# Performance work log

Hardware: AMD Instinct MI355X
Metric: run time of the kernel (lower is better)

Reference implementation:

```python
import jax, jax.numpy as jnp
import numpy as np

K = 15.0          # sigmoid sharpness in get_approxi
THETA2 = 400.0    # gaussian 'theta2' parameter
LOSS_WEIGHT = 1.0


def obb2poly_le90(boxes):
    # boxes [..., 5] = (x, y, w, h, a) -> poly [..., 8]
    x, y, w, h, a = (boxes[..., i] for i in range(5))
    cosa, sina = jnp.cos(a), jnp.sin(a)
    wx, wy = 0.5 * w * cosa, 0.5 * w * sina
    hx, hy = -0.5 * h * sina, 0.5 * h * cosa
    return jnp.stack([
        x - wx - hx, y - wy - hy,
        x + wx - hx, y + wy - hy,
        x + wx + hx, y + wy + hy,
        x - wx + hx, y - wy + hy,
    ], axis=-1)


def setup_inputs() -> dict:
    key = jax.random.key(0)
    k1, k2, k3, k4, k5, k6 = jax.random.split(key, 6)
    N, M = 256, 512

    def make_boxes(k):
        u = jax.random.uniform(k, (N, 5), dtype=jnp.float32)
        cx = 100.0 + 300.0 * u[:, 0]
        cy = 100.0 + 300.0 * u[:, 1]
        w = 20.0 + 100.0 * u[:, 2]
        h = 20.0 + 100.0 * u[:, 3]
        a = (u[:, 4] - 0.5) * (jnp.pi / 2)
        return jnp.stack([cx, cy, w, h, a], axis=-1)

    pred = make_boxes(k1)
    target = make_boxes(k2)
    mask = 512.0 * jax.random.uniform(k3, (N, M, 2), dtype=jnp.float32)
    grad_x = jax.random.normal(k4, (N, M), dtype=jnp.float32)
    grad_y = jax.random.normal(k5, (N, M), dtype=jnp.float32)
    offset = 50.0 * jax.random.uniform(k6, (N, 2), dtype=jnp.float32)
    return {"pred": pred, "target": target, "mask": mask,
            "grad_x": grad_x, "grad_y": grad_y, "offset": offset}


def _my_loss(pred, target, mask, grad_x, grad_y, offset):
    # pred/target [N,5], mask [N,M,2], grad_x/grad_y [N,M], offset [N,2]
    px = pred[:, 0] - offset[:, 0]   # [N]
    py = pred[:, 1] - offset[:, 1]
    pw, ph, pa = pred[:, 2], pred[:, 3], pred[:, 4]
    gx = target[:, 0] - offset[:, 0]
    gy = target[:, 1] - offset[:, 1]
    gw, gh, ga = target[:, 2], target[:, 3], target[:, 4]

    mx, my = mask[..., 0], mask[..., 1]            # [N,M]
    dx = mx - gx[:, None]
    dy = my - gy[:, None]
    d = jnp.sqrt(dx * dx + dy * dy)                # [N,M]
    acos_arg = jnp.clip((gx[:, None] - mx) / d, -1.0, 1.0)
    acosv = jnp.arccos(acos_arg)
    beta = jnp.where(gy[:, None] >= my, ga[:, None] + acosv, ga[:, None] - acosv)

    d_w = jnp.abs(d * jnp.cos(beta))
    d_h = jnp.abs(d * jnp.sin(beta))
    sig = jax.nn.sigmoid
    approxi_1 = (1.0 - sig(K * (d_w - gw[:, None]) / gw[:, None])) * \
                (1.0 - sig(K * (d_h - gh[:, None]) / gh[:, None]))  # [N,M]

    d_w_p = pw[:, None] * d_w / gw[:, None]
    d_h_p = ph[:, None] * d_h / gh[:, None]
    zeros = jnp.zeros_like(d_w_p)
    boxes = jnp.stack([zeros, zeros, 2.0 * d_w_p, 2.0 * d_h_p,
                       jnp.broadcast_to(pa[:, None], d_w_p.shape)], axis=-1)
    pts = obb2poly_le90(boxes)                     # [N,M,8]

    half_pi = jnp.pi / 2
    q2 = (beta > -half_pi) & (beta <= 0.0)
    q3 = (beta > -jnp.pi) & (beta <= -half_pi)
    q4 = (beta > half_pi) & (beta <= jnp.pi)
    # default (q1: 0 < beta <= pi/2) -> corner 0
    gpx = jnp.where(q2, pts[..., 2], jnp.where(q3, pts[..., 4], jnp.where(q4, pts[..., 6], pts[..., 0])))
    gpy = jnp.where(q2, pts[..., 3], jnp.where(q3, pts[..., 5], jnp.where(q4, pts[..., 7], pts[..., 1])))
    guass_x = px[:, None] + gpx                    # [N,M]
    guass_y = py[:, None] + gpy

    # approxi_2[n,i,j] = exp(+||guass_i - mask_j||^2 / (2*theta2^2)) / (2*pi*theta2)
    dgx = guass_x[:, :, None] - mx[:, None, :]
    dgy = guass_y[:, :, None] - my[:, None, :]
    approxi_2 = jnp.exp((dgx * dgx + dgy * dgy) / (2.0 * THETA2 * THETA2)) / (2.0 * jnp.pi * THETA2)

    # w[n,i,j] = gx_i*gx_j + gy_i*gy_j
    w = grad_x[:, :, None] * grad_x[:, None, :] + grad_y[:, :, None] * grad_y[:, None, :]

    loss_per_box = jnp.mean(w * approxi_2 * approxi_1[:, None, :], axis=(1, 2))  # [N]
    return loss_per_box


def reference(pred, target, mask, grad_x, grad_y, offset):
    loss_per_box = _my_loss(pred, target, mask, grad_x, grad_y, offset)
    return LOSS_WEIGHT * jnp.mean(loss_per_box)  # reduction='mean'
```

## Files before the change

### kernel.cpp

```cpp
#include <hip/hip_runtime.h>
#include <math.h>

typedef float v2f __attribute__((ext_vector_type(2)));

#define N_BOX   256
#define M_PTS   512
#define S_SPLIT 8
#define BLK_B   256
#define M2_PER  (M_PTS / S_SPLIT)
#define GRID_B  (N_BOX * S_SPLIT)


__global__ __launch_bounds__(512) void precompute(
    const float* __restrict__ pred,
    const float* __restrict__ target,
    const float* __restrict__ mask,
    const float* __restrict__ gradx,
    const float* __restrict__ grady,
    const float* __restrict__ offset,
    float4* __restrict__ P1,
    float4* __restrict__ P2)
{
    const int n = blockIdx.x;
    const int m = threadIdx.x;

    const float offx = offset[n * 2 + 0];
    const float offy = offset[n * 2 + 1];
    const float px = pred[n * 5 + 0] - offx;
    const float py = pred[n * 5 + 1] - offy;
    const float pw = pred[n * 5 + 2];
    const float ph = pred[n * 5 + 3];
    const float pa = pred[n * 5 + 4];
    const float gx = target[n * 5 + 0] - offx;
    const float gy = target[n * 5 + 1] - offy;
    const float gw = target[n * 5 + 2];
    const float gh = target[n * 5 + 3];
    const float ga = target[n * 5 + 4];

    float sinpa, cospa, singa, cosga;
    sincosf(pa, &sinpa, &cospa);
    sincosf(ga, &singa, &cosga);

    const float THETA2   = 400.0f;
    const float LOG2E    = 1.4426950408889634f;
    const float c1       = LOG2E / (2.0f * THETA2 * THETA2);
    const float rs       = sqrtf(c1);
    const float inv_norm = 1.0f / (2.0f * (float)M_PI * THETA2);

    const float pwg = pw / gw, phg = ph / gh;
    const float cwx = pwg * cospa, swx = pwg * sinpa;
    const float chx = phg * cospa, shx = phg * sinpa;
    const float absinga = fabsf(singa);
    const float kA  = 15.0f * LOG2E / gw;
    const float kH  = 15.0f * LOG2E / gh;
    const float kB  = 15.0f * LOG2E;
    const float pxrs = px * rs, pyrs = py * rs;
    const bool  gaPos = (ga > 0.0f), gaNeg = (ga < 0.0f);

    const float2* mask2 = (const float2*)mask;
    const size_t  idx   = (size_t)n * M_PTS + m;

    const float2 mp = mask2[idx];
    const float dx = mp.x - gx;
    const float dy = mp.y - gy;
    const float u = singa * dy - cosga * dx;
    const float v = -(cosga * dy + singa * dx);
    const bool sgaOk = gaPos ? (dy <= 0.0f) : (gaNeg ? (dy > 0.0f) : false);
    const bool wrap  = sgaOk && (dx > 0.0f) && (dx * absinga > fabsf(dy) * cosga);
    const float au = fabsf(u), av = fabsf(v);
    const float dws = (wrap || v > 0.0f) ? -au : au;
    const float dhs = (wrap || u > 0.0f) ? -av : av;
    const float gpx = dws * cwx - dhs * shx;
    const float gpy = dws * swx + dhs * chx;
    const float gvx = gradx[idx];
    const float gvy = grady[idx];

    const float eA = __builtin_amdgcn_exp2f(fmaf(au, kA, -kB));
    const float eB = __builtin_amdgcn_exp2f(fmaf(av, kH, -kB));
    const float B  = inv_norm / ((1.0f + eA) * (1.0f + eB));

    P1[idx] = make_float4(fmaf(gpx, rs, pxrs), fmaf(gpy, rs, pyrs), gvx, gvy);
    P2[idx] = make_float4(mp.x * rs, mp.y * rs, gvx * B, gvy * B);
}

__global__ __launch_bounds__(BLK_B, 8) void pair_sum(
    const float4* __restrict__ P1,
    const float4* __restrict__ P2,
    float* __restrict__ part)
{
    __shared__ float4 sP[M2_PER];
    const int n = blockIdx.x >> 3;
    const int s = blockIdx.x & 7;
    const int t = threadIdx.x;

    const size_t base = (size_t)n * M_PTS;
    if (t < M2_PER) sP[t] = P2[base + s * M2_PER + t];

    const float4 g0 = P1[base + t];
    const float4 g1 = P1[base + t + 256];
    __syncthreads();

    v2f Gx = {g0.x, g1.x};
    v2f Gy = {g0.y, g1.y};
    v2f accz = (v2f)0.0f, accw = (v2f)0.0f;

#pragma unroll 4
    for (int m2 = 0; m2 < M2_PER; ++m2) {
        const float4 p = sP[m2];
        v2f dgx = Gx - p.x;
        v2f dgy = Gy - p.y;
        v2f sa  = dgx * dgx + dgy * dgy;
        v2f e;
        e.x = __builtin_amdgcn_exp2f(sa.x);
        e.y = __builtin_amdgcn_exp2f(sa.y);
        accz += e * p.z;
        accw += e * p.w;
    }

    v2f gvx = {g0.z, g1.z};
    v2f gvy = {g0.w, g1.w};
    v2f tot = accz * gvx + accw * gvy;
    float acc = tot.x + tot.y;

#pragma unroll
    for (int off = 32; off > 0; off >>= 1)
        acc += __shfl_down(acc, off, 64);

    __shared__ float sW[4];
    if ((t & 63) == 0) sW[t >> 6] = acc;
    __syncthreads();
    if (t == 0) part[blockIdx.x] = sW[0] + sW[1] + sW[2] + sW[3];
}

__global__ __launch_bounds__(256) void loss_reduce(const float* __restrict__ part,
                                                   float* __restrict__ out)
{
    __shared__ float sW[4];
    const int t = threadIdx.x;
    const float4* p4 = (const float4*)part;
    const float4 a = p4[t];
    const float4 b = p4[t + 256];
    float acc = ((a.x + a.y) + (a.z + a.w)) + ((b.x + b.y) + (b.z + b.w));
#pragma unroll
    for (int off = 32; off > 0; off >>= 1)
        acc += __shfl_down(acc, off, 64);
    if ((t & 63) == 0) sW[t >> 6] = acc;
    __syncthreads();
    if (t == 0) {
        const float scale = 1.0f / ((float)N_BOX * (float)M_PTS * (float)M_PTS);
        out[0] = (sW[0] + sW[1] + sW[2] + sW[3]) * scale;
    }
}

extern "C" void kernel_launch(void* const* d_in, const int* in_sizes, int n_in,
                              void* d_out, int out_size, void* d_ws, size_t ws_size,
                              hipStream_t stream) {
    const float* pred   = (const float*)d_in[0];
    const float* target = (const float*)d_in[1];
    const float* mask   = (const float*)d_in[2];
    const float* gradx  = (const float*)d_in[3];
    const float* grady  = (const float*)d_in[4];
    const float* offset = (const float*)d_in[5];
    float* out = (float*)d_out;

    float4* P1  = (float4*)d_ws;
    float4* P2  = (float4*)((char*)d_ws + (2u << 20));
    float*  part = (float*)((char*)d_ws + (4u << 20));

    hipLaunchKernelGGL(precompute, dim3(N_BOX), dim3(M_PTS), 0, stream,
                       pred, target, mask, gradx, grady, offset, P1, P2);
    hipLaunchKernelGGL(pair_sum, dim3(GRID_B), dim3(BLK_B), 0, stream,
                       P1, P2, part);
    hipLaunchKernelGGL(loss_reduce, dim3(1), dim3(256), 0, stream, part, out);
}
```

Before: 84.01 us.

## Fuse precompute, pair sum and final reduction into one cooperative kernel

Merges the three kernels into a single cooperative launch. Each block recomputes its per-box G values and its own slice of P2 directly from the inputs, so the P1/P2 workspace round-trip disappears. The final reduction now runs after a grid-wide sync instead of in a separate kernel. To keep the grid co-resident, the split drops from 8 to 4 slices per box (1024 blocks), which doubles the inner loop per block and makes each block redundantly recompute the geometry for all 512 points.

```diff
diff --git a/kernel.cpp b/kernel.cpp
--- a/kernel.cpp
+++ b/kernel.cpp
@@ -1,28 +1,34 @@
 #include <hip/hip_runtime.h>
+#include <hip/hip_cooperative_groups.h>
 #include <math.h>
+
+namespace cg = cooperative_groups;
 
 typedef float v2f __attribute__((ext_vector_type(2)));
 
 #define N_BOX   256
 #define M_PTS   512
-#define S_SPLIT 8
-#define BLK_B   256
+#define S_SPLIT 4
+#define BLK     256
 #define M2_PER  (M_PTS / S_SPLIT)
-#define GRID_B  (N_BOX * S_SPLIT)
+#define GRID    (N_BOX * S_SPLIT)
 
-
-__global__ __launch_bounds__(512) void precompute(
+__global__ __launch_bounds__(BLK, 4) void loss_fused(
     const float* __restrict__ pred,
     const float* __restrict__ target,
     const float* __restrict__ mask,
     const float* __restrict__ gradx,
     const float* __restrict__ grady,
     const float* __restrict__ offset,
-    float4* __restrict__ P1,
-    float4* __restrict__ P2)
+    float* __restrict__ part,
+    float* __restrict__ out)
 {
-    const int n = blockIdx.x;
-    const int m = threadIdx.x;
+    __shared__ float4 sP[M2_PER];
+    __shared__ float  sW[4];
+
+    const int n = blockIdx.x >> 2;
+    const int s = blockIdx.x & 3;
+    const int t = threadIdx.x;
 
     const float offx = offset[n * 2 + 0];
     const float offy = offset[n * 2 + 1];
@@ -58,52 +64,47 @@
     const bool  gaPos = (ga > 0.0f), gaNeg = (ga < 0.0f);
 
     const float2* mask2 = (const float2*)mask;
-    const size_t  idx   = (size_t)n * M_PTS + m;
+    const size_t  base  = (size_t)n * M_PTS;
 
-    const float2 mp = mask2[idx];
-    const float dx = mp.x - gx;
-    const float dy = mp.y - gy;
-    const float u = singa * dy - cosga * dx;
-    const float v = -(cosga * dy + singa * dx);
-    const bool sgaOk = gaPos ? (dy <= 0.0f) : (gaNeg ? (dy > 0.0f) : false);
-    const bool wrap  = sgaOk && (dx > 0.0f) && (dx * absinga > fabsf(dy) * cosga);
-    const float au = fabsf(u), av = fabsf(v);
-    const float dws = (wrap || v > 0.0f) ? -au : au;
-    const float dhs = (wrap || u > 0.0f) ? -av : av;
-    const float gpx = dws * cwx - dhs * shx;
-    const float gpy = dws * swx + dhs * chx;
-    const float gvx = gradx[idx];
-    const float gvy = grady[idx];
+    if (t < M2_PER) {
+        const int m = s * M2_PER + t;
+        const float2 mp = mask2[base + m];
+        const float dx = mp.x - gx;
+        const float dy = mp.y - gy;
+        const float u = singa * dy - cosga * dx;
+        const float v = -(cosga * dy + singa * dx);
+        const float au = fabsf(u), av = fabsf(v);
+        const float eA = __builtin_amdgcn_exp2f(fmaf(au, kA, -kB));
+        const float eB = __builtin_amdgcn_exp2f(fmaf(av, kH, -kB));
+        const float B  = inv_norm / ((1.0f + eA) * (1.0f + eB));
+        sP[t] = make_float4(mp.x * rs, mp.y * rs,
+                            gradx[base + m] * B, grady[base + m] * B);
+    }
 
-    const float eA = __builtin_amdgcn_exp2f(fmaf(au, kA, -kB));
-    const float eB = __builtin_amdgcn_exp2f(fmaf(av, kH, -kB));
-    const float B  = inv_norm / ((1.0f + eA) * (1.0f + eB));
-
-    P1[idx] = make_float4(fmaf(gpx, rs, pxrs), fmaf(gpy, rs, pyrs), gvx, gvy);
-    P2[idx] = make_float4(mp.x * rs, mp.y * rs, gvx * B, gvy * B);
-}
-
-__global__ __launch_bounds__(BLK_B, 8) void pair_sum(
-    const float4* __restrict__ P1,
-    const float4* __restrict__ P2,
-    float* __restrict__ part)
-{
-    __shared__ float4 sP[M2_PER];
-    const int n = blockIdx.x >> 3;
-    const int s = blockIdx.x & 7;
-    const int t = threadIdx.x;
-
-    const size_t base = (size_t)n * M_PTS;
-    if (t < M2_PER) sP[t] = P2[base + s * M2_PER + t];
-
-    const float4 g0 = P1[base + t];
-    const float4 g1 = P1[base + t + 256];
+    v2f Gx, Gy, gvx, gvy;
+#pragma unroll
+    for (int r = 0; r < 2; ++r) {
+        const int m = t + (r << 8);
+        const float2 mp = mask2[base + m];
+        const float dx = mp.x - gx;
+        const float dy = mp.y - gy;
+        const float u = singa * dy - cosga * dx;
+        const float v = -(cosga * dy + singa * dx);
+        const bool sgaOk = gaPos ? (dy <= 0.0f) : (gaNeg ? (dy > 0.0f) : false);
+        const bool wrap  = sgaOk && (dx > 0.0f) && (dx * absinga > fabsf(dy) * cosga);
+        const float au = fabsf(u), av = fabsf(v);
+        const float dws = (wrap || v > 0.0f) ? -au : au;
+        const float dhs = (wrap || u > 0.0f) ? -av : av;
+        const float gpx = dws * cwx - dhs * shx;
+        const float gpy = dws * swx + dhs * chx;
+        Gx[r]  = fmaf(gpx, rs, pxrs);
+        Gy[r]  = fmaf(gpy, rs, pyrs);
+        gvx[r] = gradx[base + m];
+        gvy[r] = grady[base + m];
+    }
     __syncthreads();
 
-    v2f Gx = {g0.x, g1.x};
-    v2f Gy = {g0.y, g1.y};
     v2f accz = (v2f)0.0f, accw = (v2f)0.0f;
-
 #pragma unroll 4
     for (int m2 = 0; m2 < M2_PER; ++m2) {
         const float4 p = sP[m2];
@@ -117,38 +118,31 @@
         accw += e * p.w;
     }
 
-    v2f gvx = {g0.z, g1.z};
-    v2f gvy = {g0.w, g1.w};
     v2f tot = accz * gvx + accw * gvy;
     float acc = tot.x + tot.y;
-
-#pragma unroll
-    for (int off = 32; off > 0; off >>= 1)
-        acc += __shfl_down(acc, off, 64);
-
-    __shared__ float sW[4];
-    if ((t & 63) == 0) sW[t >> 6] = acc;
-    __syncthreads();
-    if (t == 0) part[blockIdx.x] = sW[0] + sW[1] + sW[2] + sW[3];
-}
-
-__global__ __launch_bounds__(256) void loss_reduce(const float* __restrict__ part,
-                                                   float* __restrict__ out)
-{
-    __shared__ float sW[4];
-    const int t = threadIdx.x;
-    const float4* p4 = (const float4*)part;
-    const float4 a = p4[t];
-    const float4 b = p4[t + 256];
-    float acc = ((a.x + a.y) + (a.z + a.w)) + ((b.x + b.y) + (b.z + b.w));
 #pragma unroll
     for (int off = 32; off > 0; off >>= 1)
         acc += __shfl_down(acc, off, 64);
     if ((t & 63) == 0) sW[t >> 6] = acc;
     __syncthreads();
-    if (t == 0) {
-        const float scale = 1.0f / ((float)N_BOX * (float)M_PTS * (float)M_PTS);
-        out[0] = (sW[0] + sW[1] + sW[2] + sW[3]) * scale;
+    if (t == 0) part[blockIdx.x] = sW[0] + sW[1] + sW[2] + sW[3];
+
+    cg::this_grid().sync();
+
+    if (blockIdx.x == 0) {
+        const float4* p4 = (const float4*)part;
+        const float4 a = p4[t];
+        float acc2 = (a.x + a.y) + (a.z + a.w);
+#pragma unroll
+        for (int off = 32; off > 0; off >>= 1)
+            acc2 += __shfl_down(acc2, off, 64);
+        __syncthreads();
+        if ((t & 63) == 0) sW[t >> 6] = acc2;
+        __syncthreads();
+        if (t == 0) {
+            const float scale = 1.0f / ((float)N_BOX * (float)M_PTS * (float)M_PTS);
+            out[0] = (sW[0] + sW[1] + sW[2] + sW[3]) * scale;
+        }
     }
 }
 
@@ -161,15 +155,11 @@
     const float* gradx  = (const float*)d_in[3];
     const float* grady  = (const float*)d_in[4];
     const float* offset = (const float*)d_in[5];
-    float* out = (float*)d_out;
+    float* out  = (float*)d_out;
+    float* part = (float*)d_ws;
 
-    float4* P1  = (float4*)d_ws;
-    float4* P2  = (float4*)((char*)d_ws + (2u << 20));
-    float*  part = (float*)((char*)d_ws + (4u << 20));
-
-    hipLaunchKernelGGL(precompute, dim3(N_BOX), dim3(M_PTS), 0, stream,
-                       pred, target, mask, gradx, grady, offset, P1, P2);
-    hipLaunchKernelGGL(pair_sum, dim3(GRID_B), dim3(BLK_B), 0, stream,
-                       P1, P2, part);
-    hipLaunchKernelGGL(loss_reduce, dim3(1), dim3(256), 0, stream, part, out);
+    void* kargs[] = { (void*)&pred, (void*)&target, (void*)&mask, (void*)&gradx,
+                      (void*)&grady, (void*)&offset, (void*)&part, (void*)&out };
+    hipLaunchCooperativeKernel((const void*)loss_fused, dim3(GRID), dim3(BLK),
+                               kargs, 0, stream);
 }
```

Result: slower. 153.2 us (+82.3%).
